# Kernel optimization log

Hardware: AMD Instinct MI355X
Metric: run time of the kernel (lower is better)

## Reference

```python
import jax, jax.numpy as jnp
import numpy as np

BRIGHT_THRESH = 0.65
SAT_THRESH = 0.15
SMOOTH_K = 15
LAMBDA_L1 = 1.0
LAMBDA_WIN_L1 = 3.0
LAMBDA_WIN_COLOR = 1.0
WINDOW_WEIGHT = 5.0
BASE_WEIGHT = 1.0
TRANSFORM_WEIGHT = 2.0
EPS = 1e-8


def _avg_pool_same(x, k=SMOOTH_K):
    # AvgPool2d(k, stride=1, padding=k//2), count_include_pad=True (torch default)
    p = k // 2
    s = jax.lax.reduce_window(x, 0.0, jax.lax.add, (1, 1, k, k), (1, 1, 1, 1),
                              [(0, 0), (0, 0), (p, p), (p, p)])
    return s / (k * k)


def _window_detector(source):
    # Rescale from [-1,1] to [0,1] if any negative values present
    src = jnp.where(source.min() < 0, (source + 1) * 0.5, source)
    brightness = 0.299 * src[:, 0:1] + 0.587 * src[:, 1:2] + 0.114 * src[:, 2:3]
    bright_mask = jax.nn.sigmoid(20.0 * (brightness - BRIGHT_THRESH))
    saturation = src.max(axis=1, keepdims=True) - src.min(axis=1, keepdims=True)
    low_sat_mask = jax.nn.sigmoid(20.0 * (SAT_THRESH - saturation))
    return _avg_pool_same(bright_mask * low_sat_mask)


def _normalize_ch(x):
    # F.normalize over channel dim with eps clamp
    n = jnp.sqrt(jnp.sum(x * x, axis=1, keepdims=True))
    return x / jnp.maximum(n, EPS)


def setup_inputs() -> dict:
    key = jax.random.key(0)
    k1, k2, k3 = jax.random.split(key, 3)
    shape = (16, 3, 512, 512)
    return {
        "pred": jax.random.normal(k1, shape, dtype=jnp.float32),
        "target": jax.random.normal(k2, shape, dtype=jnp.float32),
        "source": jax.random.normal(k3, shape, dtype=jnp.float32),
    }


def reference(pred, target, source):
    window_mask = _window_detector(source)  # [B,1,H,W]

    # plain L1
    l1_loss = jnp.abs(pred - target).mean()

    # window-weighted L1
    weight_map = BASE_WEIGHT + (WINDOW_WEIGHT - BASE_WEIGHT) * window_mask
    win_l1_loss = (jnp.abs(pred - target) * weight_map).mean()

    # window color-transform loss
    st = target - source  # source -> target direction
    sp = pred - source    # source -> pred direction
    alignment = jnp.sum(_normalize_ch(st) * _normalize_ch(sp), axis=1, keepdims=True)
    st_mag = jnp.sqrt(jnp.sum(st * st, axis=1, keepdims=True))
    sp_mag = jnp.sqrt(jnp.sum(sp * sp, axis=1, keepdims=True))
    mag_loss = jnp.abs(sp_mag / (st_mag + EPS) - 1.0)
    color_loss = TRANSFORM_WEIGHT * (window_mask * (1.0 - alignment + 0.5 * mag_loss)).mean()

    total = LAMBDA_L1 * l1_loss + LAMBDA_WIN_L1 * win_l1_loss + LAMBDA_WIN_COLOR * color_loss
    return total
```

## Files before the change

kernel.cpp:

```cpp
#include <hip/hip_runtime.h>
#include <math.h>

#define W 512
#define H 512
#define BATCH 16
#define HW (W * H)
#define NPIX (BATCH * HW)
#define NELEM (3 * NPIX)

#define TW 64
#define TH 32
#define NBLOCKS 2048

#define MROWS 46
#define MCOLS 80
#define HCOLS 64
#define HSTRIDE 68

__device__ __forceinline__ float fast_rcp(float x)  { return __builtin_amdgcn_rcpf(x); }
__device__ __forceinline__ float fast_sqrt(float x) { return __builtin_amdgcn_sqrtf(x); }

__device__ __forceinline__ float maskval(float r, float g, float b) {
    const float R = (r + 1.f) * 0.5f;
    const float G = (g + 1.f) * 0.5f;
    const float B = (b + 1.f) * 0.5f;
    const float bright = 0.299f * R + 0.587f * G + 0.114f * B;
    const float sat = fmaxf(R, fmaxf(G, B)) - fminf(R, fminf(G, B));
    const float bm = fast_rcp(1.f + __expf(-20.f * (bright - 0.65f)));
    const float sm = fast_rcp(1.f + __expf(-20.f * (0.15f - sat)));
    return bm * sm;
}

__global__ __launch_bounds__(256, 4) void k_fused(const float* __restrict__ pred,
                                                  const float* __restrict__ targ,
                                                  const float* __restrict__ srcp,
                                                  float* __restrict__ partials) {
    __shared__ __align__(16) float smask[MROWS * MCOLS];
    __shared__ __align__(16) float shsum[MROWS * HSTRIDE];

    const int tid = threadIdx.x;
    const int bid = blockIdx.x;
    const int b  = bid >> 7;
    const int tl = bid & 127;
    const int y0 = (tl >> 3) * TH;
    const int x0 = (tl & 7) * TW;
    const size_t ibase = (size_t)b * 3 * HW;

#pragma unroll
    for (int p0 = 0; p0 < 1024; p0 += 256) {
        const int p = p0 + tid;
        if (p < MROWS * 20) {
            const int r = p / 20;
            const int q = p - r * 20;
            const int gy = y0 - 7 + r;
            const int gx = x0 - 8 + 4 * q;
            float4 mv = make_float4(0.f, 0.f, 0.f, 0.f);
            if ((unsigned)gy < (unsigned)H && (unsigned)gx < (unsigned)W) {
                const size_t o = ibase + (size_t)gy * W + gx;
                const float4 R4 = *(const float4*)(srcp + o);
                const float4 G4 = *(const float4*)(srcp + o + HW);
                const float4 B4 = *(const float4*)(srcp + o + 2 * HW);
                mv.x = maskval(R4.x, G4.x, B4.x);
                mv.y = maskval(R4.y, G4.y, B4.y);
                mv.z = maskval(R4.z, G4.z, B4.z);
                mv.w = maskval(R4.w, G4.w, B4.w);
            }
            *(float4*)(smask + r * MCOLS + 4 * q) = mv;
        }
    }
    __syncthreads();

#pragma unroll
    for (int p0 = 0; p0 < MROWS * HCOLS; p0 += 256) {
        const int p = p0 + tid;
        if (p < MROWS * HCOLS) {
            const int r = p >> 6;
            const int c = p & 63;
            const float* mr = smask + r * MCOLS + c + 1;
            float s = 0.f;
#pragma unroll
            for (int k = 0; k < 15; ++k) s += mr[k];
            shsum[r * HSTRIDE + c] = s;
        }
    }
    __syncthreads();

    const int cg = tid & 15;
    const int rg = tid >> 4;
    const int ro = 2 * rg;
    const size_t base0 = ibase + (size_t)(y0 + ro) * W + (x0 + 4 * cg);
    const size_t base1 = base0 + W;

    const float4 pA0 = *(const float4*)(pred + base0);
    const float4 pB0 = *(const float4*)(pred + base0 + HW);
    const float4 pC0 = *(const float4*)(pred + base0 + 2 * HW);
    const float4 tA0 = *(const float4*)(targ + base0);
    const float4 tB0 = *(const float4*)(targ + base0 + HW);
    const float4 tC0 = *(const float4*)(targ + base0 + 2 * HW);
    const float4 sA0 = *(const float4*)(srcp + base0);
    const float4 sB0 = *(const float4*)(srcp + base0 + HW);
    const float4 sC0 = *(const float4*)(srcp + base0 + 2 * HW);
    const float4 pA1 = *(const float4*)(pred + base1);
    const float4 pB1 = *(const float4*)(pred + base1 + HW);
    const float4 pC1 = *(const float4*)(pred + base1 + 2 * HW);
    const float4 tA1 = *(const float4*)(targ + base1);
    const float4 tB1 = *(const float4*)(targ + base1 + HW);
    const float4 tC1 = *(const float4*)(targ + base1 + 2 * HW);
    const float4 sA1 = *(const float4*)(srcp + base1);
    const float4 sB1 = *(const float4*)(srcp + base1 + HW);
    const float4 sC1 = *(const float4*)(srcp + base1 + 2 * HW);

    const float* hcol = shsum + 4 * cg;
    float4 S0 = make_float4(0.f, 0.f, 0.f, 0.f);
#pragma unroll
    for (int k = 0; k < 15; ++k) {
        const float4 h = *(const float4*)(hcol + (ro + k) * HSTRIDE);
        S0.x += h.x; S0.y += h.y; S0.z += h.z; S0.w += h.w;
    }
    const float4 hsub = *(const float4*)(hcol + ro * HSTRIDE);
    const float4 hadd = *(const float4*)(hcol + (ro + 15) * HSTRIDE);
    const float4 S1 = make_float4(S0.x - hsub.x + hadd.x, S0.y - hsub.y + hadd.y,
                                  S0.z - hsub.z + hadd.z, S0.w - hsub.w + hadd.w);

    const float inv225 = 1.f / 225.f;
    float sA = 0.f, sAW = 0.f, sC = 0.f;

#pragma unroll
    for (int i = 0; i < 2; ++i) {
        const float4 Pv[3] = {i ? pA1 : pA0, i ? pB1 : pB0, i ? pC1 : pC0};
        const float4 Tv[3] = {i ? tA1 : tA0, i ? tB1 : tB0, i ? tC1 : tC0};
        const float4 Sv[3] = {i ? sA1 : sA0, i ? sB1 : sB0, i ? sC1 : sC0};
        const float4 Sw = i ? S1 : S0;
        const float wm[4] = {Sw.x * inv225, Sw.y * inv225, Sw.z * inv225, Sw.w * inv225};

        const float pr[4] = {Pv[0].x, Pv[0].y, Pv[0].z, Pv[0].w};
        const float pg[4] = {Pv[1].x, Pv[1].y, Pv[1].z, Pv[1].w};
        const float pb[4] = {Pv[2].x, Pv[2].y, Pv[2].z, Pv[2].w};
        const float tr[4] = {Tv[0].x, Tv[0].y, Tv[0].z, Tv[0].w};
        const float tg[4] = {Tv[1].x, Tv[1].y, Tv[1].z, Tv[1].w};
        const float tb[4] = {Tv[2].x, Tv[2].y, Tv[2].z, Tv[2].w};
        const float sr[4] = {Sv[0].x, Sv[0].y, Sv[0].z, Sv[0].w};
        const float sg[4] = {Sv[1].x, Sv[1].y, Sv[1].z, Sv[1].w};
        const float sb[4] = {Sv[2].x, Sv[2].y, Sv[2].z, Sv[2].w};

#pragma unroll
        for (int j = 0; j < 4; ++j) {
            const float a = fabsf(pr[j] - tr[j]) + fabsf(pg[j] - tg[j]) + fabsf(pb[j] - tb[j]);
            const float stx = tr[j] - sr[j], sty = tg[j] - sg[j], stz = tb[j] - sb[j];
            const float spx = pr[j] - sr[j], spy = pg[j] - sg[j], spz = pb[j] - sb[j];
            const float dot = stx * spx + sty * spy + stz * spz;
            const float stm = fast_sqrt(stx * stx + sty * sty + stz * stz);
            const float spm = fast_sqrt(spx * spx + spy * spy + spz * spz);
            const float align = dot * fast_rcp(fmaxf(stm, 1e-8f) * fmaxf(spm, 1e-8f));
            const float mag = fabsf(spm * fast_rcp(stm + 1e-8f) - 1.f);
            const float c = 1.f - align + 0.5f * mag;
            sA  += a;
            sAW += a * wm[j];
            sC  += c * wm[j];
        }
    }

#pragma unroll
    for (int off = 32; off > 0; off >>= 1) {
        sA  += __shfl_down(sA, off);
        sAW += __shfl_down(sAW, off);
        sC  += __shfl_down(sC, off);
    }
    __shared__ float red[3][4];
    const int lane = tid & 63;
    const int wave = tid >> 6;
    if (lane == 0) { red[0][wave] = sA; red[1][wave] = sAW; red[2][wave] = sC; }
    __syncthreads();
    if (tid == 0) {
        partials[(size_t)bid * 3 + 0] = red[0][0] + red[0][1] + red[0][2] + red[0][3];
        partials[(size_t)bid * 3 + 1] = red[1][0] + red[1][1] + red[1][2] + red[1][3];
        partials[(size_t)bid * 3 + 2] = red[2][0] + red[2][1] + red[2][2] + red[2][3];
    }
}

__global__ __launch_bounds__(256) void k_final(const float* __restrict__ partials,
                                               float* __restrict__ out) {
    double a = 0.0, aw = 0.0, c = 0.0;
    for (int i = threadIdx.x; i < NBLOCKS; i += 256) {
        a  += (double)partials[(size_t)i * 3 + 0];
        aw += (double)partials[(size_t)i * 3 + 1];
        c  += (double)partials[(size_t)i * 3 + 2];
    }
#pragma unroll
    for (int off = 32; off > 0; off >>= 1) {
        a  += __shfl_down(a, off);
        aw += __shfl_down(aw, off);
        c  += __shfl_down(c, off);
    }
    __shared__ double rd[3][4];
    const int lane = threadIdx.x & 63;
    const int wave = threadIdx.x >> 6;
    if (lane == 0) { rd[0][wave] = a; rd[1][wave] = aw; rd[2][wave] = c; }
    __syncthreads();
    if (threadIdx.x == 0) {
        const double A  = rd[0][0] + rd[0][1] + rd[0][2] + rd[0][3];
        const double AW = rd[1][0] + rd[1][1] + rd[1][2] + rd[1][3];
        const double C  = rd[2][0] + rd[2][1] + rd[2][2] + rd[2][3];
        const double N = (double)NELEM;
        const double M = (double)NPIX;
        out[0] = (float)((4.0 * A + 12.0 * AW) / N + 2.0 * C / M);
    }
}

extern "C" void kernel_launch(void* const* d_in, const int* in_sizes, int n_in,
                              void* d_out, int out_size, void* d_ws, size_t ws_size,
                              hipStream_t stream) {
    const float* pred = (const float*)d_in[0];
    const float* targ = (const float*)d_in[1];
    const float* src  = (const float*)d_in[2];

    float* partials = (float*)d_ws;

    k_fused<<<NBLOCKS, 256, 0, stream>>>(pred, targ, src, partials);
    k_final<<<1, 256, 0, stream>>>(partials, (float*)d_out);
}
```

Before: 168.6 us.

## Reuse one LDS buffer for mask and horizontal sums, vectorize sliding-window sum

```diff
diff --git a/kernel.cpp b/kernel.cpp
--- a/kernel.cpp
+++ b/kernel.cpp
@@ -16,6 +16,7 @@
 #define MCOLS 80
 #define HCOLS 64
 #define HSTRIDE 68
+#define NQUAD (MROWS * 16)
 
 __device__ __forceinline__ float fast_rcp(float x)  { return __builtin_amdgcn_rcpf(x); }
 __device__ __forceinline__ float fast_sqrt(float x) { return __builtin_amdgcn_sqrtf(x); }
@@ -31,12 +32,12 @@
     return bm * sm;
 }
 
-__global__ __launch_bounds__(256, 4) void k_fused(const float* __restrict__ pred,
+__global__ __launch_bounds__(256, 6) void k_fused(const float* __restrict__ pred,
                                                   const float* __restrict__ targ,
                                                   const float* __restrict__ srcp,
                                                   float* __restrict__ partials) {
-    __shared__ __align__(16) float smask[MROWS * MCOLS];
-    __shared__ __align__(16) float shsum[MROWS * HSTRIDE];
+    __shared__ __align__(16) float buf[MROWS * MCOLS];
+    __shared__ float red[3][4];
 
     const int tid = threadIdx.x;
     const int bid = blockIdx.x;
@@ -47,8 +48,8 @@
     const size_t ibase = (size_t)b * 3 * HW;
 
 #pragma unroll
-    for (int p0 = 0; p0 < 1024; p0 += 256) {
-        const int p = p0 + tid;
+    for (int i = 0; i < 4; ++i) {
+        const int p = i * 256 + tid;
         if (p < MROWS * 20) {
             const int r = p / 20;
             const int q = p - r * 20;
@@ -65,22 +66,43 @@
                 mv.z = maskval(R4.z, G4.z, B4.z);
                 mv.w = maskval(R4.w, G4.w, B4.w);
             }
-            *(float4*)(smask + r * MCOLS + 4 * q) = mv;
-        }
-    }
-    __syncthreads();
-
-#pragma unroll
-    for (int p0 = 0; p0 < MROWS * HCOLS; p0 += 256) {
-        const int p = p0 + tid;
-        if (p < MROWS * HCOLS) {
-            const int r = p >> 6;
-            const int c = p & 63;
-            const float* mr = smask + r * MCOLS + c + 1;
-            float s = 0.f;
-#pragma unroll
-            for (int k = 0; k < 15; ++k) s += mr[k];
-            shsum[r * HSTRIDE + c] = s;
+            *(float4*)(buf + r * MCOLS + 4 * q) = mv;
+        }
+    }
+    __syncthreads();
+
+    float4 hq[3];
+#pragma unroll
+    for (int i = 0; i < 3; ++i) {
+        const int p = i * 256 + tid;
+        if (p < NQUAD) {
+            const int r = p >> 4;
+            const int q = p & 15;
+            const float* mr = buf + r * MCOLS + 4 * q;
+            const float4 v0 = *(const float4*)(mr);
+            const float4 v1 = *(const float4*)(mr + 4);
+            const float4 v2 = *(const float4*)(mr + 8);
+            const float4 v3 = *(const float4*)(mr + 12);
+            const float4 v4 = *(const float4*)(mr + 16);
+            const float m1 = v0.y, m2 = v0.z, m3 = v0.w;
+            const float mid = v1.x + v1.y + v1.z + v1.w
+                            + v2.x + v2.y + v2.z + v2.w
+                            + v3.x + v3.y + v3.z + v3.w;
+            const float o0 = m1 + m2 + m3 + mid;
+            const float o1 = o0 - m1 + v4.x;
+            const float o2 = o1 - m2 + v4.y;
+            const float o3 = o2 - m3 + v4.z;
+            hq[i] = make_float4(o0, o1, o2, o3);
+        }
+    }
+    __syncthreads();
+#pragma unroll
+    for (int i = 0; i < 3; ++i) {
+        const int p = i * 256 + tid;
+        if (p < NQUAD) {
+            const int r = p >> 4;
+            const int q = p & 15;
+            *(float4*)(buf + r * HSTRIDE + 4 * q) = hq[i];
         }
     }
     __syncthreads();
@@ -110,7 +132,7 @@
     const float4 sB1 = *(const float4*)(srcp + base1 + HW);
     const float4 sC1 = *(const float4*)(srcp + base1 + 2 * HW);
 
-    const float* hcol = shsum + 4 * cg;
+    const float* hcol = buf + 4 * cg;
     float4 S0 = make_float4(0.f, 0.f, 0.f, 0.f);
 #pragma unroll
     for (int k = 0; k < 15; ++k) {
@@ -166,7 +188,6 @@
         sAW += __shfl_down(sAW, off);
         sC  += __shfl_down(sC, off);
     }
-    __shared__ float red[3][4];
     const int lane = tid & 63;
     const int wave = tid >> 6;
     if (lane == 0) { red[0][wave] = sA; red[1][wave] = sAW; red[2][wave] = sC; }
```

Result: no change. 166.9 us (-1.0%).
